# Performance work log

Measured on AMD Instinct MI355X. Metric: run time of the kernel, lower is better.

## Reference

```python
import jax, jax.numpy as jnp
import numpy as np
from jax import lax


def _sweep(u, w, V, axis, reverse):
    """One directional min-sum DP sweep (SGM recurrence).

    u: (B, CV, H, W, D) unary costs
    w: (B, 1, H, W)     per-pixel edge weights for this direction
    V: (D, D)           label-context (pairwise smoothness) matrix
    axis: spatial axis of u to scan along (2 = H, 3 = W)
    reverse: scan in decreasing index order
    Returns L: (B, CV, H, W, D) aggregated directional costs,
    L(p, l) = u(p, l) + min_{l'} [ L(p-d, l') + w(p) * V(l', l) ],
    with L = u at the border.
    """
    if reverse:
        u = jnp.flip(u, axis)
        w = jnp.flip(w, axis)
    u_s = jnp.moveaxis(u, axis, 0)   # (T, B, CV, P, D)
    w_s = jnp.moveaxis(w, axis, 0)   # (T, B, 1, P)

    init = u_s[0]

    def step(L_prev, xs):
        u_t, w_t = xs
        # cand[..., l', l] = L_prev[..., l'] + w_t * V[l', l]
        cand = L_prev[..., :, None] + w_t[..., None, None] * V
        L = u_t + jnp.min(cand, axis=-2)
        return L, L

    _, Ls = lax.scan(step, init, (u_s[1:], w_s[1:]))
    L_all = jnp.concatenate([init[None], Ls], axis=0)
    L_all = jnp.moveaxis(L_all, 0, axis)
    if reverse:
        L_all = jnp.flip(L_all, axis)
    return L_all


def setup_inputs() -> dict:
    key = jax.random.key(0)
    k1, k2, k3 = jax.random.split(key, 3)
    B, CV, D, H, W = 4, 1, 21, 512, 512
    N_DIR = 4
    unary = jax.random.uniform(k1, (B, CV, D, H, W), dtype=jnp.float32)
    edge_weights = jax.random.uniform(k2, (B, N_DIR, H, W), dtype=jnp.float32)
    label_context = jax.random.uniform(k3, (D, D), dtype=jnp.float32)
    return {"unary": unary, "edge_weights": edge_weights,
            "label_context": label_context}


def reference(unary, edge_weights, label_context):
    # unary: (B, CV, D, H, W) -> (B, CV, H, W, D) as in MPModule.forward
    u = jnp.transpose(unary, (0, 1, 3, 4, 2))
    # directions: 0 = left->right, 1 = right->left, 2 = top->down, 3 = bottom->up
    dir_cfg = [(3, False), (3, True), (2, False), (2, True)]
    n_dir = len(dir_cfg)
    cost = u
    for d, (axis, reverse) in enumerate(dir_cfg):
        w_d = edge_weights[:, d][:, None]  # (B, 1, H, W)
        L_d = _sweep(u, w_d, label_context, axis, reverse)
        cost = cost + (L_d - u)  # accumulate directional messages
    # permute back to (B, CV, D, H, W) as the module does
    return jnp.transpose(cost, (0, 1, 4, 2, 3))
```

## Files before the change

kernel.cpp:

```cpp
#include <hip/hip_runtime.h>


#define DLBL 21
#define SP 512
#define NB 4
#define SPSP ((long)SP * SP)
#define NELEM ((long)NB * DLBL * SP * SP)

__global__ __launch_bounds__(256)
void transpose2_kernel(const float* __restrict__ u, const float* __restrict__ ew,
                       float* __restrict__ uT, float* l2t, float* l3t)
{
    __shared__ float tile[32][33];
    const int plane = blockIdx.z;
    const float* src;
    float* dst;
    if (plane < NB * DLBL) {
        src = u  + (long)plane * SPSP;
        dst = uT + (long)plane * SPSP;
    } else {
        const int q = plane - NB * DLBL;
        const int b = q >> 1, db = q & 1;
        src = ew + (long)(b * 4 + 2 + db) * SPSP;
        dst = (db ? l3t : l2t) + (long)(b * DLBL + 20) * SPSP;
    }
    const int x0 = blockIdx.x * 32, y0 = blockIdx.y * 32;
    const int tx = threadIdx.x & 31, ty = threadIdx.x >> 5;
#pragma unroll
    for (int j = 0; j < 4; ++j)
        tile[ty + 8 * j][tx] = src[(long)(y0 + ty + 8 * j) * SP + (x0 + tx)];
    __syncthreads();
#pragma unroll
    for (int j = 0; j < 4; ++j)
        dst[(long)(x0 + ty + 8 * j) * SP + (y0 + tx)] = tile[tx][ty + 8 * j];
}

__global__ __launch_bounds__(64, 3)
void sweep3(const float* __restrict__ unary, const float* __restrict__ ew,
            const float* __restrict__ Vmat, const float* __restrict__ uT,
            float* __restrict__ out, float* __restrict__ l1,
            float* l2t, float* l3t)
{
    __shared__ float xch[4][24];
    __shared__ float stage[4][693];
    const int lane = threadIdx.x;
    const int g    = lane / DLBL;
    const int s    = lane - g * DLBL;
    int taskId = blockIdx.x * 3 + (g < 3 ? g : 0);
    if (taskId >= 8192) taskId = 8191;

    const int dir  = taskId >> 11;
    const int line = taskId & 2047;
    const int b    = line >> 9;
    const int p    = line & (SP - 1);
    const int axis = dir >> 1;
    const int rev  = dir & 1;
    const float usub = (dir == 0) ? 0.0f : 1.0f;

    float Vc[DLBL];
#pragma unroll
    for (int j = 0; j < DLBL; ++j) Vc[j] = Vmat[j * DLBL + s];

    const float4* ub4 = (const float4*)((axis ? uT : unary)
                        + (long)(b * DLBL + s) * SPSP + (long)p * SP);
    const float* wbase = axis
        ? ((dir == 2 ? l2t : l3t) + (long)(b * DLBL + 20) * SPSP + (long)p * SP)
        : (ew + (long)(b * 4 + dir) * SPSP + (long)p * SP);
    const float4* wb4 = (const float4*)wbase;

    const int frow = lane >> 5, fcol = lane & 31;
    const int stbase = s * 33;

    float4 uA[4], uB[4], wA[4], wB[4];
    float cur = 0.0f;

#define QIDX(bi, k) (rev ? (127 - 4 * (bi) - (k)) : (4 * (bi) + (k)))

#define LOADBLK(bi, U, W) do {                                              \
    _Pragma("unroll")                                                       \
    for (int k = 0; k < 4; ++k) {                                           \
        const int q_ = QIDX(bi, k);                                         \
        U[k] = ub4[q_]; W[k] = wb4[q_];                                     \
    } } while (0)

#define PROCESS(bi, U, W, FIRST) do {                                       \
    _Pragma("unroll")                                                       \
    for (int k = 0; k < 4; ++k) {                                           \
        const float ua_[4] = {U[k].x, U[k].y, U[k].z, U[k].w};              \
        const float wa_[4] = {W[k].x, W[k].y, W[k].z, W[k].w};              \
        const int q_ = QIDX(bi, k);                                         \
        _Pragma("unroll")                                                   \
        for (int j = 0; j < 4; ++j) {                                       \
            const int   jc  = rev ? 3 - j : j;                              \
            const float u_c = ua_[jc];                                      \
            const float w_c = wa_[jc];                                      \
            const int   t   = q_ * 4 + jc;                                  \
            xch[g][s] = cur;                                                \
            __builtin_amdgcn_wave_barrier();                                \
            float Lp[24];                                                   \
            _Pragma("unroll")                                               \
            for (int qq = 0; qq < 6; ++qq)                                  \
                ((float4*)Lp)[qq] = ((const float4*)(&xch[g][0]))[qq];      \
            __builtin_amdgcn_wave_barrier();                                \
            float c[DLBL];                                                  \
            _Pragma("unroll")                                               \
            for (int jj = 0; jj < DLBL; ++jj)                               \
                c[jj] = fmaf(w_c, Vc[jj], Lp[jj]);                          \
            float m7[7];                                                    \
            _Pragma("unroll")                                               \
            for (int kk = 0; kk < 7; ++kk)                                  \
                m7[kk] = fminf(fminf(c[3*kk], c[3*kk+1]), c[3*kk+2]);       \
            const float ma = fminf(fminf(m7[0], m7[1]), m7[2]);             \
            const float mb = fminf(fminf(m7[3], m7[4]), m7[5]);             \
            const float nv = u_c + fminf(fminf(ma, mb), m7[6]);             \
            cur = ((FIRST) && k == 0 && j == 0) ? u_c : nv;                 \
            stage[g][stbase + (t & 31)] = fmaf(-usub, u_c, cur);            \
        }                                                                   \
    } } while (0)

#define FLUSH(bi) do {                                                      \
    __builtin_amdgcn_wave_barrier();                                        \
    for (int gg = 0; gg < 3; ++gg) {                                        \
        const int tid = blockIdx.x * 3 + gg;                                \
        if (tid >= 8192) break;                                             \
        const int d_ = tid >> 11;                                           \
        const int ln = tid & 2047;                                          \
        const int bb = ln >> 9;                                             \
        const int pp = ln & (SP - 1);                                       \
        const int w0 = (d_ & 1) ? (496 - 16 * (bi)) : (16 * (bi) - 16);     \
        float* dst = (d_ == 0) ? out : (d_ == 1) ? l1                       \
                   : (d_ == 2) ? l2t : l3t;                                 \
        float* bp = dst + (long)(bb * DLBL) * SPSP + (long)pp * SP + w0     \
                        + (long)frow * SPSP;                                \
        _Pragma("unroll")                                                   \
        for (int r2 = 0; r2 < 11; ++r2) {                                   \
            const int rr = 2 * r2 + frow;                                   \
            if (rr < DLBL) bp[fcol] = stage[gg][rr * 33 + fcol];            \
            bp += 2 * SPSP;                                                 \
        }                                                                   \
    }                                                                       \
    __builtin_amdgcn_wave_barrier();                                        \
} while (0)

    LOADBLK(0, uA, wA);
    for (int m = 0; m < 16; ++m) {
        LOADBLK(2 * m + 1, uB, wB);
        PROCESS(2 * m, uA, wA, (m == 0));
        if (m < 15) LOADBLK(2 * m + 2, uA, wA);
        PROCESS(2 * m + 1, uB, wB, false);
        FLUSH(2 * m + 1);
    }

#undef QIDX
#undef LOADBLK
#undef PROCESS
#undef FLUSH
}

__global__ __launch_bounds__(256)
void finish_kernel(const float* __restrict__ l1, const float* __restrict__ l2t,
                   const float* __restrict__ l3t, float* __restrict__ out)
{
    __shared__ float t2[32][33], t3[32][33];
    const long pb = (long)blockIdx.z * SPSP;
    const int x0 = blockIdx.x * 32, y0 = blockIdx.y * 32;
    const int tx = threadIdx.x & 31, ty = threadIdx.x >> 5;
#pragma unroll
    for (int j = 0; j < 4; ++j) {
        const long o = pb + (long)(x0 + ty + 8 * j) * SP + (y0 + tx);
        t2[ty + 8 * j][tx] = l2t[o];
        t3[ty + 8 * j][tx] = l3t[o];
    }
    __syncthreads();
#pragma unroll
    for (int j = 0; j < 4; ++j) {
        const long o = pb + (long)(y0 + ty + 8 * j) * SP + (x0 + tx);
        out[o] = out[o] + l1[o] + t2[tx][ty + 8 * j] + t3[tx][ty + 8 * j];
    }
}

template<int MODE>
__global__ __launch_bounds__(64)
void sweep_fb(const float* __restrict__ unary, const float* __restrict__ ew,
              const float* __restrict__ Vmat, float* __restrict__ out,
              int taskBase)
{
    __shared__ float xch[4][24];
    const int lane = threadIdx.x;
    const int g    = lane / DLBL;
    const int s    = lane - g * DLBL;
    int local = blockIdx.x * 3 + (g < 3 ? g : 0);
    const bool valid = (g < 3) && (local < 2048);
    if (local >= 2048) local = 2047;
    const int taskId = taskBase + local;
    const int dir  = taskId >> 11;
    const int line = taskId & 2047;
    const int b = line >> 9, p = line & (SP - 1);
    const int axis = dir >> 1, rev = dir & 1;

    float Vc[DLBL];
#pragma unroll
    for (int j = 0; j < DLBL; ++j) Vc[j] = Vmat[j * DLBL + s];

    const long ustep = axis ? SP : 1;
    const long ubase = (long)(b * DLBL + s) * SPSP + (axis ? (long)p : (long)p * SP);
    const long wbase = (long)(b * 4 + dir) * SPSP + (axis ? (long)p : (long)p * SP);
    const long uoff  = rev ? -ustep : ustep;
    const long ust   = rev ? (long)(SP - 1) * ustep : 0;

    const float* up = unary + ubase + ust;
    const float* wp = ew    + wbase + ust;
    float*       op = out   + ubase + ust;

    float cur = up[0];
    if (valid && MODE == 1) *op = cur;

    float ub0 = up[uoff], ub1 = up[2*uoff], ub2 = up[3*uoff], ub3 = up[4*uoff];
    float wb0 = wp[uoff], wb1 = wp[2*uoff], wb2 = wp[3*uoff], wb3 = wp[4*uoff];
    float ob0 = 0, ob1 = 0, ob2 = 0, ob3 = 0;
    if (MODE == 2) { ob0 = op[uoff]; ob1 = op[2*uoff]; ob2 = op[3*uoff]; ob3 = op[4*uoff]; }
    const float* upf = up + 4 * uoff;
    const float* wpf = wp + 4 * uoff;
    const float* opf = op + 4 * uoff;

    for (int t = 1; t < SP; ++t) {
        const float u_c = ub0, w_c = wb0, o_c = ob0;
        ub0 = ub1; ub1 = ub2; ub2 = ub3;
        wb0 = wb1; wb1 = wb2; wb2 = wb3;
        if (MODE == 2) { ob0 = ob1; ob1 = ob2; ob2 = ob3; }
        const bool adv = (t + 4) < SP;
        upf += adv ? uoff : 0; wpf += adv ? uoff : 0;
        ub3 = *upf; wb3 = *wpf;
        if (MODE == 2) { opf += adv ? uoff : 0; ob3 = *opf; }

        xch[g][s] = cur;
        __builtin_amdgcn_wave_barrier();
        float Lp[24];
#pragma unroll
        for (int q = 0; q < 6; ++q)
            ((float4*)Lp)[q] = ((const float4*)(&xch[g][0]))[q];
        __builtin_amdgcn_wave_barrier();

        float c[DLBL];
#pragma unroll
        for (int j = 0; j < DLBL; ++j) c[j] = fmaf(w_c, Vc[j], Lp[j]);
        float m7[7];
#pragma unroll
        for (int k = 0; k < 7; ++k)
            m7[k] = fminf(fminf(c[3*k], c[3*k+1]), c[3*k+2]);
        const float ma = fminf(fminf(m7[0], m7[1]), m7[2]);
        const float mb = fminf(fminf(m7[3], m7[4]), m7[5]);
        cur = u_c + fminf(fminf(ma, mb), m7[6]);

        op += uoff;
        if (valid) *op = (MODE == 2) ? (o_c + cur - u_c) : cur;
    }
}

extern "C" void kernel_launch(void* const* d_in, const int* in_sizes, int n_in,
                              void* d_out, int out_size, void* d_ws, size_t ws_size,
                              hipStream_t stream) {
    const float* unary = (const float*)d_in[0];
    const float* ew    = (const float*)d_in[1];
    const float* Vmat  = (const float*)d_in[2];
    float* o = (float*)d_out;

    const size_t needA = (size_t)(4 * NELEM) * sizeof(float);

    if (ws_size >= needA) {
        float* uT  = (float*)d_ws;
        float* l1  = uT + NELEM;
        float* l2t = l1 + NELEM;
        float* l3t = l2t + NELEM;

        dim3 tg(16, 16, NB * DLBL + 8);
        transpose2_kernel<<<tg, 256, 0, stream>>>(unary, ew, uT, l2t, l3t);

        const int grid = (8192 + 2) / 3;
        sweep3<<<grid, 64, 0, stream>>>(unary, ew, Vmat, uT,
                                        o, l1, l2t, l3t);

        finish_kernel<<<dim3(16, 16, NB * DLBL), 256, 0, stream>>>(l1, l2t, l3t, o);
    } else {
        const int grid = (2048 + 2) / 3;
        sweep_fb<1><<<grid, 64, 0, stream>>>(unary, ew, Vmat, o, 0);
        for (int d = 1; d < 4; ++d)
            sweep_fb<2><<<grid, 64, 0, stream>>>(unary, ew, Vmat, o, d * 2048);
    }
}
```

Before: 449.0 us.

## Deepen sweep load pipeline to four blocks and precompute flush addresses

The sweep kernel now keeps four in-flight register buffers of unary and weight loads instead of two, so global loads are issued further ahead of the serial DP recurrence. Per-task output base pointers and direction flags are computed once before the loop rather than inside every flush. This is meant to hide more global memory latency and trim address arithmetic in the flush path. The cost is double the register use for staged loads, which risks spilling or lower occupancy under the 64-thread, 3-block launch bounds.

After: 554.9 us. 1.24x slower.

```diff
diff --git a/kernel.cpp b/kernel.cpp
--- a/kernel.cpp
+++ b/kernel.cpp
@@ -36,7 +36,7 @@
 }
 
 __global__ __launch_bounds__(64, 3)
-void sweep3(const float* __restrict__ unary, const float* __restrict__ ew,
+void sweep4(const float* __restrict__ unary, const float* __restrict__ ew,
             const float* __restrict__ Vmat, const float* __restrict__ uT,
             float* __restrict__ out, float* __restrict__ l1,
             float* l2t, float* l3t)
@@ -71,19 +71,38 @@
     const int frow = lane >> 5, fcol = lane & 31;
     const int stbase = s * 33;
 
-    float4 uA[4], uB[4], wA[4], wB[4];
+    float* fb[3]; int wrev[3]; bool fvalid[3];
+#pragma unroll
+    for (int gg = 0; gg < 3; ++gg) {
+        const int tid = blockIdx.x * 3 + gg;
+        fvalid[gg] = (tid < 8192);
+        const int tid2 = fvalid[gg] ? tid : 8191;
+        const int d_ = tid2 >> 11;
+        const int ln = tid2 & 2047;
+        const int bb = ln >> 9;
+        const int pp = ln & (SP - 1);
+        wrev[gg] = d_ & 1;
+        float* dst = (d_ == 0) ? out : (d_ == 1) ? l1 : (d_ == 2) ? l2t : l3t;
+        fb[gg] = dst + (long)(bb * DLBL) * SPSP + (long)pp * SP + (long)frow * SPSP;
+    }
+
+    float4 uS0[4], uS1[4], uS2[4], uS3[4];
+    float4 wS0[4], wS1[4], wS2[4], wS3[4];
     float cur = 0.0f;
 
 #define QIDX(bi, k) (rev ? (127 - 4 * (bi) - (k)) : (4 * (bi) + (k)))
 
-#define LOADBLK(bi, U, W) do {                                              \
+#define LOADU(bi, U) do {                                                   \
     _Pragma("unroll")                                                       \
-    for (int k = 0; k < 4; ++k) {                                           \
-        const int q_ = QIDX(bi, k);                                         \
-        U[k] = ub4[q_]; W[k] = wb4[q_];                                     \
-    } } while (0)
-
-#define PROCESS(bi, U, W, FIRST) do {                                       \
+    for (int k = 0; k < 4; ++k) U[k] = ub4[QIDX(bi, k)];                    \
+    } while (0)
+
+#define LOADW(bi, W) do {                                                   \
+    _Pragma("unroll")                                                       \
+    for (int k = 0; k < 4; ++k) W[k] = wb4[QIDX(bi, k)];                    \
+    } while (0)
+
+#define PROC(bi, U, W, FIRSTB) do {                                         \
     _Pragma("unroll")                                                       \
     for (int k = 0; k < 4; ++k) {                                           \
         const float ua_[4] = {U[k].x, U[k].y, U[k].z, U[k].w};              \
@@ -113,48 +132,53 @@
             const float ma = fminf(fminf(m7[0], m7[1]), m7[2]);             \
             const float mb = fminf(fminf(m7[3], m7[4]), m7[5]);             \
             const float nv = u_c + fminf(fminf(ma, mb), m7[6]);             \
-            cur = ((FIRST) && k == 0 && j == 0) ? u_c : nv;                 \
+            cur = ((FIRSTB) && k == 0 && j == 0) ? u_c : nv;                \
             stage[g][stbase + (t & 31)] = fmaf(-usub, u_c, cur);            \
         }                                                                   \
     } } while (0)
 
-#define FLUSH(bi) do {                                                      \
+#define FLW(w_) do {                                                        \
     __builtin_amdgcn_wave_barrier();                                        \
+    _Pragma("unroll")                                                       \
     for (int gg = 0; gg < 3; ++gg) {                                        \
-        const int tid = blockIdx.x * 3 + gg;                                \
-        if (tid >= 8192) break;                                             \
-        const int d_ = tid >> 11;                                           \
-        const int ln = tid & 2047;                                          \
-        const int bb = ln >> 9;                                             \
-        const int pp = ln & (SP - 1);                                       \
-        const int w0 = (d_ & 1) ? (496 - 16 * (bi)) : (16 * (bi) - 16);     \
-        float* dst = (d_ == 0) ? out : (d_ == 1) ? l1                       \
-                   : (d_ == 2) ? l2t : l3t;                                 \
-        float* bp = dst + (long)(bb * DLBL) * SPSP + (long)pp * SP + w0     \
-                        + (long)frow * SPSP;                                \
-        _Pragma("unroll")                                                   \
-        for (int r2 = 0; r2 < 11; ++r2) {                                   \
-            const int rr = 2 * r2 + frow;                                   \
-            if (rr < DLBL) bp[fcol] = stage[gg][rr * 33 + fcol];            \
-            bp += 2 * SPSP;                                                 \
+        if (fvalid[gg]) {                                                   \
+            float* bp = fb[gg] + (wrev[gg] ? (480 - 32 * (w_))              \
+                                           : (32 * (w_)));                  \
+            _Pragma("unroll")                                               \
+            for (int r2 = 0; r2 < 11; ++r2) {                               \
+                const int rr = 2 * r2 + frow;                               \
+                if (rr < DLBL) bp[fcol] = stage[gg][rr * 33 + fcol];        \
+                bp += 2 * SPSP;                                             \
+            }                                                               \
         }                                                                   \
     }                                                                       \
     __builtin_amdgcn_wave_barrier();                                        \
 } while (0)
 
-    LOADBLK(0, uA, wA);
-    for (int m = 0; m < 16; ++m) {
-        LOADBLK(2 * m + 1, uB, wB);
-        PROCESS(2 * m, uA, wA, (m == 0));
-        if (m < 15) LOADBLK(2 * m + 2, uA, wA);
-        PROCESS(2 * m + 1, uB, wB, false);
-        FLUSH(2 * m + 1);
+    LOADU(0, uS0); LOADW(0, wS0);
+    LOADU(1, uS1); LOADW(1, wS1);
+    LOADU(2, uS2); LOADW(2, wS2);
+    LOADU(3, uS3); LOADW(3, wS3);
+
+    for (int ww = 0; ww < 8; ++ww) {
+        const int B0 = 4 * ww;
+        PROC(B0 + 0, uS0, wS0, (ww == 0));
+        if (B0 + 4 < 32) { LOADU(B0 + 4, uS0); LOADW(B0 + 4, wS0); }
+        PROC(B0 + 1, uS1, wS1, false);
+        if (B0 + 5 < 32) { LOADU(B0 + 5, uS1); LOADW(B0 + 5, wS1); }
+        FLW(2 * ww);
+        PROC(B0 + 2, uS2, wS2, false);
+        if (B0 + 6 < 32) { LOADU(B0 + 6, uS2); LOADW(B0 + 6, wS2); }
+        PROC(B0 + 3, uS3, wS3, false);
+        if (B0 + 7 < 32) { LOADU(B0 + 7, uS3); LOADW(B0 + 7, wS3); }
+        FLW(2 * ww + 1);
     }
 
 #undef QIDX
-#undef LOADBLK
-#undef PROCESS
-#undef FLUSH
+#undef LOADU
+#undef LOADW
+#undef PROC
+#undef FLW
 }
 
 __global__ __launch_bounds__(256)
@@ -277,7 +301,7 @@
         transpose2_kernel<<<tg, 256, 0, stream>>>(unary, ew, uT, l2t, l3t);
 
         const int grid = (8192 + 2) / 3;
-        sweep3<<<grid, 64, 0, stream>>>(unary, ew, Vmat, uT,
+        sweep4<<<grid, 64, 0, stream>>>(unary, ew, Vmat, uT,
                                         o, l1, l2t, l3t);
 
         finish_kernel<<<dim3(16, 16, NB * DLBL), 256, 0, stream>>>(l1, l2t, l3t, o);
```
